# Kernel tuning notes

Measured on AMD Instinct MI355X. Metric: run time of the kernel, lower is better.

## Reference

```python
import jax, jax.numpy as jnp
import numpy as np

B, N, E, FIN, H, D = 256, 1024, 8192, 8, 4, 5
HD = H * D            # GATv2: 4 heads * 5 dim, concat -> 20
OBS = N               # flattened obs length
AOUT = 64             # action_space_output_dim (aggregator output)
HID = 256             # hidden_size
NOUT = 64             # num_outputs (logits)
NEG = 0.2             # GATv2 leaky_relu negative slope
EPS = 1e-5            # batchnorm eps


def setup_inputs() -> dict:
    key = jax.random.key(0)
    ks = jax.random.split(key, 16)
    def lin(k, i, o):
        return (jax.random.normal(k, (i, o), jnp.float32) / np.sqrt(i)).astype(jnp.float32)
    return {
        "x": jax.random.normal(ks[0], (B, N, FIN), jnp.float32),
        "obs": jax.random.normal(ks[1], (B, OBS), jnp.float32),
        "edge_index": jax.random.randint(ks[2], (2, E), 0, N),
        # GATv2 layer 0 (in=FIN) and layer 1 (in=HD)
        "Wl0": lin(ks[3], FIN, HD), "Wr0": lin(ks[4], FIN, HD),
        "att0": (jax.random.normal(ks[5], (H, D), jnp.float32) * 0.1), "b0": jnp.zeros((HD,), jnp.float32),
        "Wl1": lin(ks[6], HD, HD), "Wr1": lin(ks[7], HD, HD),
        "att1": (jax.random.normal(ks[8], (H, D), jnp.float32) * 0.1), "b1": jnp.zeros((HD,), jnp.float32),
        # BatchNorm params per layer (over feature dim)
        "g0": jnp.ones((HD,), jnp.float32), "be0": jnp.zeros((HD,), jnp.float32),
        "g1": jnp.ones((HD,), jnp.float32), "be1": jnp.zeros((HD,), jnp.float32),
        # aggregator linear (mean pool -> action-space dim)
        "Wagg": lin(ks[9], HD, AOUT), "bagg": jnp.zeros((AOUT,), jnp.float32),
        # logits MLP: cat(agg, obs) -> HID -> HID//2 -> NOUT (tanh activations)
        "W1": lin(ks[10], AOUT + OBS, HID), "bh1": jnp.zeros((HID,), jnp.float32),
        "W2": lin(ks[11], HID, HID // 2), "bh2": jnp.zeros((HID // 2,), jnp.float32),
        "Wout": lin(ks[12], HID // 2, NOUT), "bout": jnp.zeros((NOUT,), jnp.float32),
    }


def _gatv2_single(x, src, dst, Wl, Wr, att, bias):
    # x: [N, Fin]; src/dst: [Es] (with self loops)
    xl = (x @ Wl).reshape(N, H, D)
    xr = (x @ Wr).reshape(N, H, D)
    m = jax.nn.leaky_relu(xl[src] + xr[dst], NEG)        # [Es, H, D]
    e = jnp.einsum('ehd,hd->eh', m, att)                 # [Es, H]
    emax = jax.ops.segment_max(e, dst, num_segments=N)   # every node has a self loop
    p = jnp.exp(e - emax[dst])
    s = jax.ops.segment_sum(p, dst, num_segments=N)
    alpha = p / s[dst]                                   # softmax over incoming edges
    out = jax.ops.segment_sum(alpha[:, :, None] * xl[src], dst, num_segments=N)
    return out.reshape(N, HD) + bias


def _bn(x, g, b):
    # training-mode batchnorm over all (batch, node) positions, per feature
    mu = x.mean(axis=(0, 1))
    var = x.var(axis=(0, 1))
    return (x - mu) * jax.lax.rsqrt(var + EPS) * g + b


def reference(x, obs, edge_index, Wl0, Wr0, att0, b0, Wl1, Wr1, att1, b1,
              g0, be0, g1, be1, Wagg, bagg, W1, bh1, W2, bh2, Wout, bout):
    loops = jnp.arange(N)
    src = jnp.concatenate([edge_index[0], loops])
    dst = jnp.concatenate([edge_index[1], loops])
    layer = lambda xb, Wl, Wr, att, bias: jax.vmap(
        lambda xn: _gatv2_single(xn, src, dst, Wl, Wr, att, bias))(xb)
    h = layer(x, Wl0, Wr0, att0, b0)       # [B, N, HD]
    h = _bn(h, g0, be0)
    h = layer(h, Wl1, Wr1, att1, b1)
    h = _bn(h, g1, be1)
    agg = h.mean(axis=1) @ Wagg + bagg     # mean graph pooling -> [B, AOUT]
    f = jnp.concatenate([agg, obs], axis=1)
    f = jnp.tanh(f @ W1 + bh1)
    f = jnp.tanh(f @ W2 + bh2)
    return f @ Wout + bout                 # logits [B, NOUT]
```

## Files before the change

### kernel.cpp

```cpp
#include <hip/hip_runtime.h>
#include <hip/hip_bf16.h>
#include <math.h>

typedef unsigned short u16;
typedef __attribute__((ext_vector_type(8))) short short8;
typedef __attribute__((ext_vector_type(4))) float floatx4;

constexpr int kN   = 1024;
constexpr int kB   = 256;
constexpr int kE   = 8192;
constexpr int kHD  = 20;
constexpr float kEps = 1e-5f;

static __device__ __forceinline__ float u16_bf16_to_f32(u16 v) {
  return __uint_as_float(((unsigned)v) << 16);
}
static __device__ __forceinline__ void unpack2(unsigned u, float& a, float& b) {
  a = __uint_as_float(u << 16);
  b = __uint_as_float(u & 0xffff0000u);
}
static __device__ __forceinline__ u16 f2bf(float f) {
  __hip_bfloat16 h = __float2bfloat16(f);
  return *reinterpret_cast<u16*>(&h);
}
static __device__ __forceinline__ unsigned pack_bf16(float a, float b) {
  return (unsigned)f2bf(a) | ((unsigned)f2bf(b) << 16);
}

static __device__ __forceinline__ int detect_flag(const unsigned* __restrict__ x) {
  unsigned w = x[threadIdx.x & 63];
  unsigned e = (w >> 7) & 0xFFu;
  bool plaus = (e >= 114u && e <= 136u);
  unsigned long long b = __ballot(plaus);
  return (__popcll(b) >= 32) ? 1 : 0;
}
static __device__ __forceinline__ float ldconv(const void* __restrict__ p, int i, int flag) {
  return flag ? u16_bf16_to_f32(((const u16*)p)[i]) : ((const float*)p)[i];
}

static __device__ __forceinline__ void repack_one(const void* __restrict__ src,
                                                  u16* __restrict__ dst,
                                                  int c, int N, int srcbf) {
  int n = c % N;
  int t2 = c / N;
  int q = t2 & 3, kb = t2 >> 2;
  int k0 = kb * 32 + q * 8;
  u16 w[8];
  if (srcbf) {
    const u16* s = (const u16*)src;
#pragma unroll
    for (int j = 0; j < 8; j++) w[j] = s[(size_t)(k0 + j) * N + n];
  } else {
    const float* s = (const float*)src;
#pragma unroll
    for (int j = 0; j < 8; j++) w[j] = f2bf(s[(size_t)(k0 + j) * N + n]);
  }
  uint4 out;
  out.x = (unsigned)w[0] | ((unsigned)w[1] << 16);
  out.y = (unsigned)w[2] | ((unsigned)w[3] << 16);
  out.z = (unsigned)w[4] | ((unsigned)w[5] << 16);
  out.w = (unsigned)w[6] | ((unsigned)w[7] << 16);
  *((uint4*)(dst + (size_t)c * 8)) = out;
}

__global__ __launch_bounds__(1024) void setup_kernel(
    const unsigned* __restrict__ xdet,
    const void* __restrict__ xin,
    const int* __restrict__ ei,
    const void* __restrict__ Wl0, const void* __restrict__ Wr0,
    const void* __restrict__ W1, const void* __restrict__ W2, const void* __restrict__ Wout,
    int* __restrict__ csr_off, int* __restrict__ csr_src,
    float* __restrict__ sums,
    u16* __restrict__ W1p, u16* __restrict__ W2p, u16* __restrict__ Woutp,
    u16* __restrict__ xlb, u16* __restrict__ xrb) {
  int bid = blockIdx.x;
  int t = threadIdx.x;
  if (bid == 0) {
    __shared__ int cnt[kN];
    __shared__ int tmp[kN];
    __shared__ int cur[kN];
    cnt[t] = 0;
    __syncthreads();
    for (int e = t; e < kE; e += 1024) atomicAdd(&cnt[ei[kE + e]], 1);
    __syncthreads();
    int deg = cnt[t] + 1;
    tmp[t] = deg;
    __syncthreads();
    for (int o = 1; o < kN; o <<= 1) {
      int add = (t >= o) ? tmp[t - o] : 0;
      __syncthreads();
      tmp[t] += add;
      __syncthreads();
    }
    int excl = tmp[t] - deg;
    csr_off[t] = excl;
    cur[t] = excl;
    if (t == kN - 1) csr_off[kN] = tmp[t];
    __syncthreads();
    for (int e = t; e < kE; e += 1024) {
      int s = ei[e], d2 = ei[kE + e];
      int pos = atomicAdd(&cur[d2], 1);
      csr_src[pos] = s;
    }
    int pos = atomicAdd(&cur[t], 1);
    csr_src[pos] = t;
    if (t < 640) sums[t] = 0.f;
  } else if (bid <= 39) {
    int flag = detect_flag(xdet);
    int c = (bid - 1) * 1024 + t;
    if (c < 34816) repack_one(W1, W1p, c, 256, flag);
    else if (c < 38912) repack_one(W2, W2p, c - 34816, 128, flag);
    else repack_one(Wout, Woutp, c - 38912, 64, flag);
  } else {
    int flag = detect_flag(xdet);
    __shared__ __align__(16) float wl[8 * kHD], wr[8 * kHD];
    if (t < 8 * kHD) { wl[t] = ldconv(Wl0, t, flag); wr[t] = ldconv(Wr0, t, flag); }
    __syncthreads();
    int n = (bid - 40) * 4 + (t >> 8), b = t & 255;
    float xi[8];
    if (flag) {
      uint4 r = *((const uint4*)((const u16*)xin + ((size_t)b * kN + n) * 8));
      unpack2(r.x, xi[0], xi[1]); unpack2(r.y, xi[2], xi[3]);
      unpack2(r.z, xi[4], xi[5]); unpack2(r.w, xi[6], xi[7]);
    } else {
      const float4* s = (const float4*)((const float*)xin + ((size_t)b * kN + n) * 8);
      float4 v0 = s[0], v1 = s[1];
      xi[0] = v0.x; xi[1] = v0.y; xi[2] = v0.z; xi[3] = v0.w;
      xi[4] = v1.x; xi[5] = v1.y; xi[6] = v1.z; xi[7] = v1.w;
    }
    float ol[kHD], orr[kHD];
#pragma unroll
    for (int j = 0; j < kHD; j++) { ol[j] = 0.f; orr[j] = 0.f; }
#pragma unroll
    for (int i = 0; i < 8; i++) {
      float xv = xi[i];
#pragma unroll
      for (int j4 = 0; j4 < 5; j4++) {
        float4 wv = *((const float4*)&wl[i * kHD + j4 * 4]);
        float4 wu = *((const float4*)&wr[i * kHD + j4 * 4]);
        ol[j4 * 4 + 0] = fmaf(xv, wv.x, ol[j4 * 4 + 0]);
        ol[j4 * 4 + 1] = fmaf(xv, wv.y, ol[j4 * 4 + 1]);
        ol[j4 * 4 + 2] = fmaf(xv, wv.z, ol[j4 * 4 + 2]);
        ol[j4 * 4 + 3] = fmaf(xv, wv.w, ol[j4 * 4 + 3]);
        orr[j4 * 4 + 0] = fmaf(xv, wu.x, orr[j4 * 4 + 0]);
        orr[j4 * 4 + 1] = fmaf(xv, wu.y, orr[j4 * 4 + 1]);
        orr[j4 * 4 + 2] = fmaf(xv, wu.z, orr[j4 * 4 + 2]);
        orr[j4 * 4 + 3] = fmaf(xv, wu.w, orr[j4 * 4 + 3]);
      }
    }
    uint2* pl = (uint2*)(xlb + ((size_t)n * kB + b) * kHD);
    uint2* pr = (uint2*)(xrb + ((size_t)n * kB + b) * kHD);
#pragma unroll
    for (int k = 0; k < 5; k++) {
      pl[k] = make_uint2(pack_bf16(ol[4 * k], ol[4 * k + 1]), pack_bf16(ol[4 * k + 2], ol[4 * k + 3]));
      pr[k] = make_uint2(pack_bf16(orr[4 * k], orr[4 * k + 1]), pack_bf16(orr[4 * k + 2], orr[4 * k + 3]));
    }
  }
}

__global__ __launch_bounds__(128) void attn_kernel(const u16* __restrict__ xlb,
                                                   const u16* __restrict__ xrb,
                                                   const int* __restrict__ csr_off,
                                                   const int* __restrict__ csr_src,
                                                   const void* __restrict__ attraw,
                                                   const void* __restrict__ braw,
                                                   const unsigned* __restrict__ xdet,
                                                   u16* __restrict__ hout,
                                                   float* __restrict__ sums) {
  __shared__ float satt[kHD], sbias[kHD];
  __shared__ float red[2][2 * kHD];
  int flag = detect_flag(xdet);
  int t = threadIdx.x;
  if (t < kHD) { satt[t] = ldconv(attraw, t, flag); sbias[t] = ldconv(braw, t, flag); }
  __syncthreads();
  int bid = blockIdx.x;
  int h = ((bid & 7) >= 4) ? 1 : 0;
  int n = ((bid >> 3) << 2) | (bid & 3);
  int b = (h << 7) | t;

  float ratt[kHD];
#pragma unroll
  for (int f = 0; f < kHD; f++) ratt[f] = satt[f];

  float xrv[kHD];
  {
    const uint2* p = (const uint2*)(xrb + ((size_t)n * kB + b) * kHD);
#pragma unroll
    for (int k = 0; k < 5; k++) {
      uint2 v = p[k];
      unpack2(v.x, xrv[4 * k], xrv[4 * k + 1]);
      unpack2(v.y, xrv[4 * k + 2], xrv[4 * k + 3]);
    }
  }
  float s[4] = {0.f, 0.f, 0.f, 0.f};
  float acc[kHD];
#pragma unroll
  for (int f = 0; f < kHD; f++) acc[f] = 0.f;

  int beg = csr_off[n], end = csr_off[n + 1];
  uint2 r[5];
  {
    const uint2* p = (const uint2*)(xlb + ((size_t)csr_src[beg] * kB + b) * kHD);
#pragma unroll
    for (int k = 0; k < 5; k++) r[k] = p[k];
  }
  for (int idx = beg; idx < end; idx++) {
    float xs[kHD];
#pragma unroll
    for (int k = 0; k < 5; k++) {
      unpack2(r[k].x, xs[4 * k], xs[4 * k + 1]);
      unpack2(r[k].y, xs[4 * k + 2], xs[4 * k + 3]);
    }
    if (idx + 1 < end) {
      const uint2* p = (const uint2*)(xlb + ((size_t)csr_src[idx + 1] * kB + b) * kHD);
#pragma unroll
      for (int k = 0; k < 5; k++) r[k] = p[k];
    }
#pragma unroll
    for (int hh = 0; hh < 4; hh++) {
      float e = 0.f;
#pragma unroll
      for (int d = 0; d < 5; d++) {
        int f = hh * 5 + d;
        float v = xs[f] + xrv[f];
        v = fmaxf(v, 0.2f * v);
        e = fmaf(v, ratt[f], e);
      }
      float p = __expf(e);
      s[hh] += p;
#pragma unroll
      for (int d = 0; d < 5; d++) {
        int f = hh * 5 + d;
        acc[f] = fmaf(p, xs[f], acc[f]);
      }
    }
  }
  float hv[kHD];
#pragma unroll
  for (int hh = 0; hh < 4; hh++) {
    float inv = 1.f / s[hh];
#pragma unroll
    for (int d = 0; d < 5; d++) {
      int f = hh * 5 + d;
      hv[f] = fmaf(acc[f], inv, sbias[f]);
    }
  }
  {
    uint2* ph = (uint2*)(hout + ((size_t)n * kB + b) * kHD);
#pragma unroll
    for (int k = 0; k < 5; k++)
      ph[k] = make_uint2(pack_bf16(hv[4 * k], hv[4 * k + 1]), pack_bf16(hv[4 * k + 2], hv[4 * k + 3]));
  }
  int lane = t & 63, wv = t >> 6;
#pragma unroll
  for (int f = 0; f < kHD; f++) {
    float a = hv[f], q = hv[f] * hv[f];
    for (int o = 32; o > 0; o >>= 1) { a += __shfl_down(a, o); q += __shfl_down(q, o); }
    if (lane == 0) { red[wv][f] = a; red[wv][kHD + f] = q; }
  }
  __syncthreads();
  if (t < 2 * kHD) atomicAdd(&sums[(bid & 7) * 2 * kHD + t], red[0][t] + red[1][t]);
}

__global__ __launch_bounds__(256) void lin1_kernel(const u16* __restrict__ hb,
                                                   const float* __restrict__ sums0,
                                                   const void* __restrict__ g0,
                                                   const void* __restrict__ be0,
                                                   const void* __restrict__ Wl1,
                                                   const void* __restrict__ Wr1,
                                                   const unsigned* __restrict__ xdet,
                                                   u16* __restrict__ xlb,
                                                   u16* __restrict__ xrb) {
  __shared__ __align__(16) float wl[kHD * kHD], wr[kHD * kHD];
  __shared__ float sbl[kHD], sbr[kHD];
  __shared__ float sa[kHD], sc[kHD], tot[2 * kHD];
  int flag = detect_flag(xdet);
  int t = threadIdx.x;
  if (t < 2 * kHD) {
    float v = 0.f;
    for (int k = 0; k < 8; k++) v += sums0[k * 2 * kHD + t];
    tot[t] = v;
  }
  __syncthreads();
  if (t < kHD) {
    const float inv = 1.0f / (float)(kN * kB);
    float mu = tot[t] * inv;
    float var = tot[kHD + t] * inv - mu * mu;
    float av = ldconv(g0, t, flag) * rsqrtf(var + kEps);
    sa[t] = av;
    sc[t] = ldconv(be0, t, flag) - mu * av;
  }
  __syncthreads();
  for (int idx = t; idx < kHD * kHD; idx += 256) {
    int f = idx / kHD;
    wl[idx] = sa[f] * ldconv(Wl1, idx, flag);
    wr[idx] = sa[f] * ldconv(Wr1, idx, flag);
  }
  if (t < kHD) {
    float sl = 0.f, sr = 0.f;
    for (int f = 0; f < kHD; f++) {
      sl += sc[f] * ldconv(Wl1, f * kHD + t, flag);
      sr += sc[f] * ldconv(Wr1, f * kHD + t, flag);
    }
    sbl[t] = sl;
    sbr[t] = sr;
  }
  __syncthreads();
  int n = blockIdx.x, b = t;
  float hv[kHD];
  {
    const uint2* p = (const uint2*)(hb + ((size_t)n * kB + b) * kHD);
#pragma unroll
    for (int k = 0; k < 5; k++) {
      uint2 v = p[k];
      unpack2(v.x, hv[4 * k], hv[4 * k + 1]);
      unpack2(v.y, hv[4 * k + 2], hv[4 * k + 3]);
    }
  }
  float ol[kHD], orr[kHD];
#pragma unroll
  for (int j = 0; j < kHD; j++) { ol[j] = sbl[j]; orr[j] = sbr[j]; }
#pragma unroll
  for (int f = 0; f < kHD; f++) {
    float xv = hv[f];
#pragma unroll
    for (int j4 = 0; j4 < 5; j4++) {
      float4 wv = *((const float4*)&wl[f * kHD + j4 * 4]);
      float4 wu = *((const float4*)&wr[f * kHD + j4 * 4]);
      ol[j4 * 4 + 0] = fmaf(xv, wv.x, ol[j4 * 4 + 0]);
      ol[j4 * 4 + 1] = fmaf(xv, wv.y, ol[j4 * 4 + 1]);
      ol[j4 * 4 + 2] = fmaf(xv, wv.z, ol[j4 * 4 + 2]);
      ol[j4 * 4 + 3] = fmaf(xv, wv.w, ol[j4 * 4 + 3]);
      orr[j4 * 4 + 0] = fmaf(xv, wu.x, orr[j4 * 4 + 0]);
      orr[j4 * 4 + 1] = fmaf(xv, wu.y, orr[j4 * 4 + 1]);
      orr[j4 * 4 + 2] = fmaf(xv, wu.z, orr[j4 * 4 + 2]);
      orr[j4 * 4 + 3] = fmaf(xv, wu.w, orr[j4 * 4 + 3]);
    }
  }
  uint2* pl = (uint2*)(xlb + ((size_t)n * kB + b) * kHD);
  uint2* pr = (uint2*)(xrb + ((size_t)n * kB + b) * kHD);
#pragma unroll
  for (int k = 0; k < 5; k++) {
    pl[k] = make_uint2(pack_bf16(ol[4 * k], ol[4 * k + 1]), pack_bf16(ol[4 * k + 2], ol[4 * k + 3]));
    pr[k] = make_uint2(pack_bf16(orr[4 * k], orr[4 * k + 1]), pack_bf16(orr[4 * k + 2], orr[4 * k + 3]));
  }
}

__global__ __launch_bounds__(256) void pool_fin_kernel(const u16* __restrict__ hb,
                                                       const float* __restrict__ sums1,
                                                       const void* __restrict__ g1,
                                                       const void* __restrict__ be1,
                                                       const void* __restrict__ Wagg,
                                                       const void* __restrict__ bagg,
                                                       const void* __restrict__ obsraw,
                                                       const unsigned* __restrict__ xdet,
                                                       u16* __restrict__ finb) {
  int flag = detect_flag(xdet);
  int b = blockIdx.x, t = threadIdx.x;
  float acc[kHD];
#pragma unroll
  for (int f = 0; f < kHD; f++) acc[f] = 0.f;
  for (int n = t; n < kN; n += 256) {
    const uint2* p = (const uint2*)(hb + ((size_t)n * kB + b) * kHD);
#pragma unroll
    for (int k = 0; k < 5; k++) {
      uint2 v = p[k];
      float a0, a1, a2, a3;
      unpack2(v.x, a0, a1); unpack2(v.y, a2, a3);
      acc[4 * k] += a0; acc[4 * k + 1] += a1; acc[4 * k + 2] += a2; acc[4 * k + 3] += a3;
    }
  }
  __shared__ float red[4][kHD];
  __shared__ float tot[2 * kHD], pv[kHD];
#pragma unroll
  for (int f = 0; f < kHD; f++) {
    float v = acc[f];
    for (int o = 32; o > 0; o >>= 1) v += __shfl_down(v, o);
    if ((t & 63) == 0) red[t >> 6][f] = v;
  }
  if (t < 2 * kHD) {
    float v = 0.f;
    for (int k = 0; k < 8; k++) v += sums1[k * 2 * kHD + t];
    tot[t] = v;
  }
  __syncthreads();
  if (t < kHD) {
    const float inv = 1.0f / (float)(kN * kB);
    float mu = tot[t] * inv;
    float var = tot[kHD + t] * inv - mu * mu;
    float a1 = ldconv(g1, t, flag) * rsqrtf(var + kEps);
    float c1 = ldconv(be1, t, flag) - mu * a1;
    float pool = (red[0][t] + red[1][t] + red[2][t] + red[3][t]) * (1.0f / kN);
    pv[t] = pool * a1 + c1;
  }
  __syncthreads();
  if (t < 64) {
    float agg = ldconv(bagg, t, flag);
#pragma unroll
    for (int f = 0; f < kHD; f++) agg = fmaf(pv[f], ldconv(Wagg, f * 64 + t, flag), agg);
    finb[(size_t)b * 1088 + t] = f2bf(agg);
  }
  if (t < 128) {
    uint4* dst = (uint4*)(finb + (size_t)b * 1088 + 64 + t * 8);
    if (flag) {
      *dst = *((const uint4*)((const u16*)obsraw + (size_t)b * 1024 + t * 8));
    } else {
      const float4* s = (const float4*)((const float*)obsraw + (size_t)b * 1024 + t * 8);
      float4 r0 = s[0], r1 = s[1];
      uint4 o;
      o.x = pack_bf16(r0.x, r0.y); o.y = pack_bf16(r0.z, r0.w);
      o.z = pack_bf16(r1.x, r1.y); o.w = pack_bf16(r1.z, r1.w);
      *dst = o;
    }
  }
}

__global__ __launch_bounds__(256) void mlp1_kernel(const u16* __restrict__ finb,
                                                   const u16* __restrict__ W1p,
                                                   const void* __restrict__ bh1,
                                                   const unsigned* __restrict__ xdet,
                                                   u16* __restrict__ h1b) {
  int flag = detect_flag(xdet);
  int tid = threadIdx.x;
  int wave = tid >> 6, lane = tid & 63;
  int tile = blockIdx.x * 4 + wave;
  int m0 = (tile >> 4) << 4, n0 = (tile & 15) << 4;
  int lo = lane & 15, quad = lane >> 4;
  floatx4 acc = {0.f, 0.f, 0.f, 0.f};
  const u16* ap = finb + (size_t)(m0 + lo) * 1088 + quad * 8;
  const u16* bp = W1p + ((size_t)quad * 256 + n0 + lo) * 8;
  for (int kb = 0; kb < 34; kb++) {
    short8 a = *(const short8*)ap; ap += 32;
    short8 bfr = *(const short8*)bp; bp += 4 * 256 * 8;
    acc = __builtin_amdgcn_mfma_f32_16x16x32_bf16(a, bfr, acc, 0, 0, 0);
  }
  float bias = ldconv(bh1, n0 + lo, flag);
  u16* op = h1b + (size_t)(m0 + quad * 4) * 256 + n0 + lo;
#pragma unroll
  for (int r = 0; r < 4; r++) op[r * 256] = f2bf(tanhf(acc[r] + bias));
}

__global__ __launch_bounds__(256) void mlp23_kernel(const u16* __restrict__ h1b,
                                                    const u16* __restrict__ W2p,
                                                    const u16* __restrict__ Woutp,
                                                    const void* __restrict__ bh2,
                                                    const void* __restrict__ bout,
                                                    const unsigned* __restrict__ xdet,
                                                    void* __restrict__ outv) {
  __shared__ __align__(16) u16 h2s[16][128];
  int flag = detect_flag(xdet);
  int tid = threadIdx.x;
  int wave = tid >> 6, lane = tid & 63;
  int lo = lane & 15, quad = lane >> 4;
  int m0 = blockIdx.x * 16;
#pragma unroll
  for (int i = 0; i < 2; i++) {
    int n0 = (wave * 2 + i) * 16;
    floatx4 acc = {0.f, 0.f, 0.f, 0.f};
    const u16* ap = h1b + (size_t)(m0 + lo) * 256 + quad * 8;
    const u16* bp = W2p + ((size_t)quad * 128 + n0 + lo) * 8;
    for (int kb = 0; kb < 8; kb++) {
      short8 a = *(const short8*)ap; ap += 32;
      short8 bfr = *(const short8*)bp; bp += 4 * 128 * 8;
      acc = __builtin_amdgcn_mfma_f32_16x16x32_bf16(a, bfr, acc, 0, 0, 0);
    }
    float bias = ldconv(bh2, n0 + lo, flag);
#pragma unroll
    for (int r = 0; r < 4; r++) h2s[quad * 4 + r][n0 + lo] = f2bf(tanhf(acc[r] + bias));
  }
  __syncthreads();
  {
    int n0 = wave * 16;
    floatx4 acc = {0.f, 0.f, 0.f, 0.f};
    const u16* bp = Woutp + ((size_t)quad * 64 + n0 + lo) * 8;
    for (int kb = 0; kb < 4; kb++) {
      short8 a = *(const short8*)(&h2s[lo][kb * 32 + quad * 8]);
      short8 bfr = *(const short8*)bp; bp += 4 * 64 * 8;
      acc = __builtin_amdgcn_mfma_f32_16x16x32_bf16(a, bfr, acc, 0, 0, 0);
    }
    float bias = ldconv(bout, n0 + lo, flag);
    if (flag) {
      __hip_bfloat16* o = (__hip_bfloat16*)outv;
#pragma unroll
      for (int r = 0; r < 4; r++)
        o[(size_t)(m0 + quad * 4 + r) * 64 + n0 + lo] = __float2bfloat16(acc[r] + bias);
    } else {
      float* o = (float*)outv;
#pragma unroll
      for (int r = 0; r < 4; r++)
        o[(size_t)(m0 + quad * 4 + r) * 64 + n0 + lo] = acc[r] + bias;
    }
  }
}

extern "C" void kernel_launch(void* const* d_in, const int* in_sizes, int n_in,
                              void* d_out, int out_size, void* d_ws, size_t ws_size,
                              hipStream_t stream) {
  char* ws = (char*)d_ws;
  float* sums    = (float*)(ws + 0);
  float* sums0   = sums;
  float* sums1   = sums + 320;
  int*   csr_off = (int*)(ws + 2560);
  int*   csr_src = (int*)(ws + 6912);
  u16*   W1p     = (u16*)(ws + 44032);
  u16*   W2p     = (u16*)(ws + 601088);
  u16*   Woutp   = (u16*)(ws + 666624);
  u16*   h1b     = (u16*)(ws + 683008);
  u16*   finb    = (u16*)(ws + 814080);
  u16*   xlb     = (u16*)(ws + 1371136);
  u16*   xrb     = (u16*)(ws + 11856896);
  u16*   hb      = (u16*)(ws + 22342656);

  const unsigned* xdet = (const unsigned*)d_in[0];
  const int* ei = (const int*)d_in[2];

  setup_kernel<<<296, 1024, 0, stream>>>(xdet, d_in[0], ei,
                                         d_in[3], d_in[4],
                                         d_in[17], d_in[19], d_in[21],
                                         csr_off, csr_src, sums,
                                         W1p, W2p, Woutp, xlb, xrb);
  attn_kernel<<<2 * kN, 128, 0, stream>>>(xlb, xrb, csr_off, csr_src,
                                          d_in[5], d_in[6], xdet, hb, sums0);
  lin1_kernel<<<kN, 256, 0, stream>>>(hb, sums0, d_in[11], d_in[12],
                                      d_in[7], d_in[8], xdet, xlb, xrb);
  attn_kernel<<<2 * kN, 128, 0, stream>>>(xlb, xrb, csr_off, csr_src,
                                          d_in[9], d_in[10], xdet, hb, sums1);
  pool_fin_kernel<<<kB, 256, 0, stream>>>(hb, sums1, d_in[13], d_in[14],
                                          d_in[15], d_in[16], d_in[1], xdet, finb);
  mlp1_kernel<<<64, 256, 0, stream>>>(finb, W1p, d_in[18], xdet, h1b);
  mlp23_kernel<<<16, 256, 0, stream>>>(h1b, W2p, Woutp, d_in[20], d_in[22], xdet, d_out);
}
```

Before: 212.2 us.

## Split BN fold into tiny kernel and run layer-1 projections with bf16 MFMA

The per-block BN-folding of Wl1/Wr1 is moved into a single-block kernel that writes packed bf16 B-fragments and a fused bias vector once. The layer-1 linear projection then uses 16x16x32 bf16 MFMA instructions over 16-row tiles instead of per-thread scalar FMAs. This removes 1024 redundant weight-folding setups and offloads the projection math to matrix cores. The trade-offs are an extra kernel launch, bf16 rounding of the folded weights, and scattered 2-byte stores for the outputs.

```diff
diff --git a/kernel.cpp b/kernel.cpp
--- a/kernel.cpp
+++ b/kernel.cpp
@@ -262,17 +262,14 @@
   if (t < 2 * kHD) atomicAdd(&sums[(bid & 7) * 2 * kHD + t], red[0][t] + red[1][t]);
 }
 
-__global__ __launch_bounds__(256) void lin1_kernel(const u16* __restrict__ hb,
-                                                   const float* __restrict__ sums0,
-                                                   const void* __restrict__ g0,
-                                                   const void* __restrict__ be0,
-                                                   const void* __restrict__ Wl1,
-                                                   const void* __restrict__ Wr1,
-                                                   const unsigned* __restrict__ xdet,
-                                                   u16* __restrict__ xlb,
-                                                   u16* __restrict__ xrb) {
-  __shared__ __align__(16) float wl[kHD * kHD], wr[kHD * kHD];
-  __shared__ float sbl[kHD], sbr[kHD];
+__global__ __launch_bounds__(256) void fold1_kernel(const float* __restrict__ sums0,
+                                                    const void* __restrict__ g0,
+                                                    const void* __restrict__ be0,
+                                                    const void* __restrict__ Wl1,
+                                                    const void* __restrict__ Wr1,
+                                                    const unsigned* __restrict__ xdet,
+                                                    u16* __restrict__ Bp,
+                                                    float* __restrict__ bias48) {
   __shared__ float sa[kHD], sc[kHD], tot[2 * kHD];
   int flag = detect_flag(xdet);
   int t = threadIdx.x;
@@ -291,58 +288,80 @@
     sc[t] = ldconv(be0, t, flag) - mu * av;
   }
   __syncthreads();
-  for (int idx = t; idx < kHD * kHD; idx += 256) {
-    int f = idx / kHD;
-    wl[idx] = sa[f] * ldconv(Wl1, idx, flag);
-    wr[idx] = sa[f] * ldconv(Wr1, idx, flag);
-  }
-  if (t < kHD) {
-    float sl = 0.f, sr = 0.f;
-    for (int f = 0; f < kHD; f++) {
-      sl += sc[f] * ldconv(Wl1, f * kHD + t, flag);
-      sr += sc[f] * ldconv(Wr1, f * kHD + t, flag);
-    }
-    sbl[t] = sl;
-    sbr[t] = sr;
-  }
-  __syncthreads();
-  int n = blockIdx.x, b = t;
-  float hv[kHD];
-  {
-    const uint2* p = (const uint2*)(hb + ((size_t)n * kB + b) * kHD);
-#pragma unroll
-    for (int k = 0; k < 5; k++) {
-      uint2 v = p[k];
-      unpack2(v.x, hv[4 * k], hv[4 * k + 1]);
-      unpack2(v.y, hv[4 * k + 2], hv[4 * k + 3]);
-    }
-  }
-  float ol[kHD], orr[kHD];
-#pragma unroll
-  for (int j = 0; j < kHD; j++) { ol[j] = sbl[j]; orr[j] = sbr[j]; }
-#pragma unroll
-  for (int f = 0; f < kHD; f++) {
-    float xv = hv[f];
-#pragma unroll
-    for (int j4 = 0; j4 < 5; j4++) {
-      float4 wv = *((const float4*)&wl[f * kHD + j4 * 4]);
-      float4 wu = *((const float4*)&wr[f * kHD + j4 * 4]);
-      ol[j4 * 4 + 0] = fmaf(xv, wv.x, ol[j4 * 4 + 0]);
-      ol[j4 * 4 + 1] = fmaf(xv, wv.y, ol[j4 * 4 + 1]);
-      ol[j4 * 4 + 2] = fmaf(xv, wv.z, ol[j4 * 4 + 2]);
-      ol[j4 * 4 + 3] = fmaf(xv, wv.w, ol[j4 * 4 + 3]);
-      orr[j4 * 4 + 0] = fmaf(xv, wu.x, orr[j4 * 4 + 0]);
-      orr[j4 * 4 + 1] = fmaf(xv, wu.y, orr[j4 * 4 + 1]);
-      orr[j4 * 4 + 2] = fmaf(xv, wu.z, orr[j4 * 4 + 2]);
-      orr[j4 * 4 + 3] = fmaf(xv, wu.w, orr[j4 * 4 + 3]);
-    }
-  }
-  uint2* pl = (uint2*)(xlb + ((size_t)n * kB + b) * kHD);
-  uint2* pr = (uint2*)(xrb + ((size_t)n * kB + b) * kHD);
-#pragma unroll
-  for (int k = 0; k < 5; k++) {
-    pl[k] = make_uint2(pack_bf16(ol[4 * k], ol[4 * k + 1]), pack_bf16(ol[4 * k + 2], ol[4 * k + 3]));
-    pr[k] = make_uint2(pack_bf16(orr[4 * k], orr[4 * k + 1]), pack_bf16(orr[4 * k + 2], orr[4 * k + 3]));
+  if (t < 48) {
+    float bv = 0.f;
+    if (t < 20) {
+      for (int f = 0; f < kHD; f++) bv += sc[f] * ldconv(Wl1, f * kHD + t, flag);
+    } else if (t < 40) {
+      for (int f = 0; f < kHD; f++) bv += sc[f] * ldconv(Wr1, f * kHD + (t - 20), flag);
+    }
+    bias48[t] = bv;
+  }
+  if (t >= 64 && t < 64 + 192) {
+    int c = t - 64;
+    int ncol = c % 48, q = c / 48;
+    u16 w[8];
+#pragma unroll
+    for (int jj = 0; jj < 8; jj++) {
+      int k = q * 8 + jj;
+      float val = 0.f;
+      if (k < kHD && ncol < 40) {
+        float raw = (ncol < kHD) ? ldconv(Wl1, k * kHD + ncol, flag)
+                                 : ldconv(Wr1, k * kHD + (ncol - 20), flag);
+        val = sa[k] * raw;
+      }
+      w[jj] = f2bf(val);
+    }
+    uint4 out;
+    out.x = (unsigned)w[0] | ((unsigned)w[1] << 16);
+    out.y = (unsigned)w[2] | ((unsigned)w[3] << 16);
+    out.z = (unsigned)w[4] | ((unsigned)w[5] << 16);
+    out.w = (unsigned)w[6] | ((unsigned)w[7] << 16);
+    *((uint4*)(Bp + (size_t)c * 8)) = out;
+  }
+}
+
+__global__ __launch_bounds__(256) void lin1_mfma_kernel(const u16* __restrict__ hb,
+                                                        const u16* __restrict__ Bp,
+                                                        const float* __restrict__ bias48,
+                                                        u16* __restrict__ xlb,
+                                                        u16* __restrict__ xrb) {
+  int tid = threadIdx.x;
+  int wave = tid >> 6, lane = tid & 63;
+  int lo = lane & 15, quad = lane >> 4;
+  short8 bfr0 = *(const short8*)(Bp + ((size_t)(quad * 48 + 0 + lo)) * 8);
+  short8 bfr1 = *(const short8*)(Bp + ((size_t)(quad * 48 + 16 + lo)) * 8);
+  short8 bfr2 = *(const short8*)(Bp + ((size_t)(quad * 48 + 32 + lo)) * 8);
+  float bc0 = bias48[lo], bc1 = bias48[16 + lo], bc2 = bias48[32 + lo];
+  int wtile0 = (blockIdx.x * 4 + wave) * 8;
+  for (int it = 0; it < 8; it++) {
+    int m0 = (wtile0 + it) << 4;
+    const uint2* p = (const uint2*)(hb + (size_t)(m0 + lo) * kHD);
+    uint2 w0 = p[0], w1 = p[1], w2 = p[2], w3 = p[3], w4 = p[4];
+    unsigned aw0 = quad == 0 ? w0.x : quad == 1 ? w2.x : quad == 2 ? w4.x : 0u;
+    unsigned aw1 = quad == 0 ? w0.y : quad == 1 ? w2.y : quad == 2 ? w4.y : 0u;
+    unsigned aw2 = quad == 0 ? w1.x : quad == 1 ? w3.x : 0u;
+    unsigned aw3 = quad == 0 ? w1.y : quad == 1 ? w3.y : 0u;
+    union { unsigned u[4]; short8 s; } cvt;
+    cvt.u[0] = aw0; cvt.u[1] = aw1; cvt.u[2] = aw2; cvt.u[3] = aw3;
+    short8 a = cvt.s;
+    floatx4 acc0 = {0.f, 0.f, 0.f, 0.f};
+    floatx4 acc1 = {0.f, 0.f, 0.f, 0.f};
+    floatx4 acc2 = {0.f, 0.f, 0.f, 0.f};
+    acc0 = __builtin_amdgcn_mfma_f32_16x16x32_bf16(a, bfr0, acc0, 0, 0, 0);
+    acc1 = __builtin_amdgcn_mfma_f32_16x16x32_bf16(a, bfr1, acc1, 0, 0, 0);
+    acc2 = __builtin_amdgcn_mfma_f32_16x16x32_bf16(a, bfr2, acc2, 0, 0, 0);
+#pragma unroll
+    for (int r = 0; r < 4; r++) {
+      size_t row = (size_t)(m0 + quad * 4 + r);
+      xlb[row * kHD + lo] = f2bf(acc0[r] + bc0);
+      int c1 = 16 + lo;
+      float v1 = acc1[r] + bc1;
+      if (c1 < kHD) xlb[row * kHD + c1] = f2bf(v1);
+      else xrb[row * kHD + (c1 - kHD)] = f2bf(v1);
+      int c2 = 12 + lo;
+      if (c2 < kHD) xrb[row * kHD + c2] = f2bf(acc2[r] + bc2);
+    }
   }
 }
 
@@ -507,9 +526,11 @@
   u16*   Woutp   = (u16*)(ws + 666624);
   u16*   h1b     = (u16*)(ws + 683008);
   u16*   finb    = (u16*)(ws + 814080);
-  u16*   xlb     = (u16*)(ws + 1371136);
-  u16*   xrb     = (u16*)(ws + 11856896);
-  u16*   hb      = (u16*)(ws + 22342656);
+  u16*   Bp      = (u16*)(ws + 1371136);
+  float* bias48  = (float*)(ws + 1374208);
+  u16*   xlb     = (u16*)(ws + 1374720);
+  u16*   xrb     = (u16*)(ws + 11860480);
+  u16*   hb      = (u16*)(ws + 22346240);
 
   const unsigned* xdet = (const unsigned*)d_in[0];
   const int* ei = (const int*)d_in[2];
@@ -521,8 +542,9 @@
                                          W1p, W2p, Woutp, xlb, xrb);
   attn_kernel<<<2 * kN, 128, 0, stream>>>(xlb, xrb, csr_off, csr_src,
                                           d_in[5], d_in[6], xdet, hb, sums0);
-  lin1_kernel<<<kN, 256, 0, stream>>>(hb, sums0, d_in[11], d_in[12],
-                                      d_in[7], d_in[8], xdet, xlb, xrb);
+  fold1_kernel<<<1, 256, 0, stream>>>(sums0, d_in[11], d_in[12],
+                                      d_in[7], d_in[8], xdet, Bp, bias48);
+  lin1_mfma_kernel<<<512, 256, 0, stream>>>(hb, Bp, bias48, xlb, xrb);
   attn_kernel<<<2 * kN, 128, 0, stream>>>(xlb, xrb, csr_off, csr_src,
                                           d_in[9], d_in[10], xdet, hb, sums1);
   pool_fin_kernel<<<kB, 256, 0, stream>>>(hb, sums1, d_in[13], d_in[14],
```

After: 211.5 us. Within noise of the previous version (-0.3%).
